# Kernel optimization log

Hardware: AMD Instinct MI355X
Metric: run time of the kernel (lower is better)

The kernel has to match this reference:

```python
import jax, jax.numpy as jnp
import numpy as np

H2 = 450
W = 1242
H = 375
N_PTS = 4_000_000


def setup_inputs() -> dict:
    key = jax.random.key(0)
    k1, k2, k3, k4, k5 = jax.random.split(key, 5)
    # lidar point cloud in velodyne frame (homogeneous): x forward, y left, z up
    u = jax.random.uniform(k1, (N_PTS, 3), dtype=jnp.float32)
    x = u[:, 0] * 78.0 + 2.0           # 2..80 m forward
    y = (u[:, 1] - 0.5) * 40.0         # -20..20 m lateral
    z = (u[:, 2] - 0.5) * 4.0 - 1.0    # -3..1 m vertical
    velo = jnp.stack([x, y, z, jnp.ones_like(x)], axis=1)
    # KITTI-like padded 4x4 intrinsic
    intrinsic = jnp.array([[721.5, 0.0, 609.5, 0.0],
                           [0.0, 721.5, 172.8, 0.0],
                           [0.0, 0.0, 1.0, 0.0],
                           [0.0, 0.0, 0.0, 1.0]], dtype=jnp.float32)
    # cam extrinsic ~ identity with small stereo baseline translation
    camExtrinsic = jnp.eye(4, dtype=jnp.float32).at[0, 3].set(-0.06)
    # velodyne -> camera rigid transform
    R = jnp.array([[0.0, -1.0, 0.0],
                   [0.0, 0.0, -1.0],
                   [1.0, 0.0, 0.0]], dtype=jnp.float32)
    t = jnp.array([0.0, -0.08, -0.27], dtype=jnp.float32)
    lidarExtrinsic = jnp.eye(4, dtype=jnp.float32).at[:3, :3].set(R).at[:3, 3].set(t)
    d = jax.random.uniform(k2, (H2, W), dtype=jnp.float32) * 78.0 + 2.0
    sel = jax.random.uniform(k3, (H2, W), dtype=jnp.float32) > 0.3
    interp_depth = jnp.where(sel, d, 0.0)
    return {"velo": velo, "intrinsic": intrinsic, "camExtrinsic": camExtrinsic,
            "lidarExtrinsic": lidarExtrinsic, "interp_depth": interp_depth,
            "h": H, "w": W}


def reference(velo, intrinsic, camExtrinsic, lidarExtrinsic, interp_depth, h, w):
    h2, wd = interp_depth.shape
    n = velo.shape[0]
    f32 = interp_depth.dtype

    P_cam = intrinsic @ camExtrinsic      # 4x4 projection to camera image
    P_lid = intrinsic @ lidarExtrinsic    # 4x4 projection to lidar image

    # project points into camera image
    vp = velo @ P_cam.T                    # [N,4]
    vz = vp[:, 2]
    vx = vp[:, 0] / vz
    vy = vp[:, 1] / vz
    onimg = (velo[:, 0] > 0) & (vx > 0) & (vx < w) & (vy > 0) & (vy < h)

    # project points into lidar image
    nv = velo @ P_lid.T                    # [N,4]
    nz = nv[:, 2]
    nx = nv[:, 0] / nz
    ny = nv[:, 1] / nz
    rnx = jnp.round(nx).astype(jnp.int32)
    rny = jnp.round(ny).astype(jnp.int32)
    nval = (rnx >= 0) & (rnx < w) & (rny >= 0) & (rny < h2) & (nz > 0) & onimg

    # dense interp-depth backprojection / reprojection, [h2, w]
    xxx, yyy = jnp.meshgrid(jnp.arange(wd, dtype=f32), jnp.arange(h2, dtype=f32), indexing='xy')
    d = interp_depth
    pts = jnp.stack([xxx * d, yyy * d, d, jnp.ones_like(d)], axis=-1)  # [h2,w,4]
    M = P_cam @ jnp.linalg.inv(P_lid)
    pp = jnp.einsum('hwk,jk->hwj', pts, M)                              # [h2,w,4]
    ppz = pp[..., 2]
    ppz_safe = jnp.where(ppz != 0, ppz, 1.0)
    ppx = pp[..., 0] / ppz_safe
    ppy = pp[..., 1] / ppz_safe
    interp_vals = jnp.stack([xxx, yyy, d, ppx, ppy, ppz, jnp.zeros_like(d)], axis=-1)
    img = jnp.where((d > 0)[..., None], interp_vals, 0.0)               # [h2,w,7]

    # scatter lidar points (overwrites interp entries where both present)
    idxrec = jnp.arange(n, dtype=f32)
    pvals = jnp.stack([nx, ny, nz, vx, vy, vz, idxrec], axis=1)         # [N,7]
    y_safe = jnp.where(nval, rny, h2)                                   # OOB -> dropped
    img = img.at[y_safe, rnx].set(pvals, mode='drop')

    org_mask = jnp.zeros((h2, wd), dtype=f32).at[y_safe, rnx].set(1.0, mode='drop')
    # NOTE: the custom CUDA occlusion pass (LidarFilterCuda.lidar_denoise) is
    # not reproducible; reference keeps the pre-denoise mask (identity filter).
    noocc_mask = org_mask

    pt_idx = img[:, :, 6].astype(jnp.int32)
    keep = noocc_mask == 1
    fi_idx = jnp.where(keep, pt_idx, n)                                 # OOB -> dropped
    filterIndicator = jnp.zeros((n,), dtype=jnp.int32).at[fi_idx.reshape(-1)].set(1, mode='drop')

    return img, noocc_mask, org_mask, filterIndicator
```

## Files before the change

kernel.cpp:

```cpp
#include <hip/hip_runtime.h>

#define H2C 450
#define WC 1242
#define HC 375
#define NPTS 4000000
#define NPIX (H2C * WC)


__device__ __forceinline__ void mm4(float* o, const float* a, const float* b) {
    for (int i = 0; i < 4; i++)
        for (int j = 0; j < 4; j++) {
            float t = a[i * 4 + 0] * b[0 * 4 + j];
            t = fmaf(a[i * 4 + 1], b[1 * 4 + j], t);
            t = fmaf(a[i * 4 + 2], b[2 * 4 + j], t);
            t = fmaf(a[i * 4 + 3], b[3 * 4 + j], t);
            o[i * 4 + j] = t;
        }
}

__global__ void setup_k(const float* __restrict__ K, const float* __restrict__ C,
                        const float* __restrict__ L, float* __restrict__ mats) {
#pragma clang fp contract(off)
    if (threadIdx.x != 0 || blockIdx.x != 0) return;
    float Pc[16], Pl[16], A[16], X[16], M[16];
    mm4(Pc, K, C);
    mm4(Pl, K, L);
    for (int i = 0; i < 16; i++) A[i] = Pl[i];
    int piv[4];
    for (int k = 0; k < 4; k++) {
        int p = k; float mx = fabsf(A[k * 4 + k]);
        for (int i = k + 1; i < 4; i++) { float v = fabsf(A[i * 4 + k]); if (v > mx) { mx = v; p = i; } }
        piv[k] = p;
        if (p != k) for (int j = 0; j < 4; j++) { float t = A[k * 4 + j]; A[k * 4 + j] = A[p * 4 + j]; A[p * 4 + j] = t; }
        float akk = A[k * 4 + k];
        if (fabsf(akk) >= 1.17549435e-38f) {
            float r = 1.0f / akk;
            for (int i = k + 1; i < 4; i++) A[i * 4 + k] = A[i * 4 + k] * r;
        } else {
            for (int i = k + 1; i < 4; i++) A[i * 4 + k] = A[i * 4 + k] / akk;
        }
        for (int i = k + 1; i < 4; i++) {
            float lik = A[i * 4 + k];
            for (int j = k + 1; j < 4; j++) A[i * 4 + j] = A[i * 4 + j] - lik * A[k * 4 + j];
        }
    }
    for (int i = 0; i < 16; i++) X[i] = 0.0f;
    X[0] = X[5] = X[10] = X[15] = 1.0f;
    for (int k = 0; k < 4; k++) if (piv[k] != k)
        for (int j = 0; j < 4; j++) { float t = X[k * 4 + j]; X[k * 4 + j] = X[piv[k] * 4 + j]; X[piv[k] * 4 + j] = t; }
    for (int j = 0; j < 4; j++) {
        for (int k = 0; k < 4; k++) {
            float xk = X[k * 4 + j];
            for (int i = k + 1; i < 4; i++) X[i * 4 + j] = X[i * 4 + j] - xk * A[i * 4 + k];
        }
        for (int k = 3; k >= 0; k--) {
            float xk = X[k * 4 + j] / A[k * 4 + k];
            X[k * 4 + j] = xk;
            for (int i = 0; i < k; i++) X[i * 4 + j] = X[i * 4 + j] - xk * A[i * 4 + k];
        }
    }
    mm4(M, Pc, X);
    for (int i = 0; i < 16; i++) { mats[i] = Pc[i]; mats[16 + i] = Pl[i]; mats[32 + i] = M[i]; }
}

__global__ void init_k(float4* __restrict__ fi4, int4* __restrict__ winner4) {
    int i = blockIdx.x * blockDim.x + threadIdx.x;
    if (i < NPTS / 4) fi4[i] = make_float4(0.f, 0.f, 0.f, 0.f);
    if (i < NPIX / 4) winner4[i] = make_int4(-1, -1, -1, -1);
}

__global__ void point_k(const float4* __restrict__ velo, const float* __restrict__ mats,
                        int* __restrict__ winner) {
    int i = blockIdx.x * blockDim.x + threadIdx.x;
    if (i >= NPTS) return;
    float4 v = velo[i];
    const float* Pc = mats;
    const float* Pl = mats + 16;
    float vp0 = fmaf(v.w, Pc[3],  fmaf(v.z, Pc[2],  fmaf(v.y, Pc[1], v.x * Pc[0])));
    float vp1 = fmaf(v.w, Pc[7],  fmaf(v.z, Pc[6],  fmaf(v.y, Pc[5], v.x * Pc[4])));
    float vz  = fmaf(v.w, Pc[11], fmaf(v.z, Pc[10], fmaf(v.y, Pc[9], v.x * Pc[8])));
    float vx = vp0 / vz;
    float vy = vp1 / vz;
    bool onimg = (v.x > 0.f) && (vx > 0.f) && (vx < (float)WC) && (vy > 0.f) && (vy < (float)HC);
    float nv0 = fmaf(v.w, Pl[3],  fmaf(v.z, Pl[2],  fmaf(v.y, Pl[1], v.x * Pl[0])));
    float nv1 = fmaf(v.w, Pl[7],  fmaf(v.z, Pl[6],  fmaf(v.y, Pl[5], v.x * Pl[4])));
    float nz  = fmaf(v.w, Pl[11], fmaf(v.z, Pl[10], fmaf(v.y, Pl[9], v.x * Pl[8])));
    float nx = nv0 / nz;
    float ny = nv1 / nz;
    float rx = rintf(nx);
    float ry = rintf(ny);
    if (onimg && (nz > 0.f) && (rx >= 0.f) && (rx < (float)WC) && (ry >= 0.f) && (ry < (float)H2C)) {
        int px = (int)rx, py = (int)ry;
        atomicMax(&winner[py * WC + px], i);
    }
}

__global__ void resolve_k(const float* __restrict__ depth, const float4* __restrict__ velo,
                          const float* __restrict__ mats, const int* __restrict__ winner,
                          float* __restrict__ img, float* __restrict__ noocc,
                          float* __restrict__ org, float* __restrict__ fi) {
#pragma clang fp contract(off)
    int p = blockIdx.x * blockDim.x + threadIdx.x;
    if (p >= NPIX) return;
    int wi = winner[p];
    float o0, o1, o2, o3, o4, o5, o6;
    if (wi >= 0) {
        float4 v = velo[wi];
        const float* Pc = mats;
        const float* Pl = mats + 16;
        float vp0 = fmaf(v.w, Pc[3],  fmaf(v.z, Pc[2],  fmaf(v.y, Pc[1], v.x * Pc[0])));
        float vp1 = fmaf(v.w, Pc[7],  fmaf(v.z, Pc[6],  fmaf(v.y, Pc[5], v.x * Pc[4])));
        float vz  = fmaf(v.w, Pc[11], fmaf(v.z, Pc[10], fmaf(v.y, Pc[9], v.x * Pc[8])));
        float nv0 = fmaf(v.w, Pl[3],  fmaf(v.z, Pl[2],  fmaf(v.y, Pl[1], v.x * Pl[0])));
        float nv1 = fmaf(v.w, Pl[7],  fmaf(v.z, Pl[6],  fmaf(v.y, Pl[5], v.x * Pl[4])));
        float nz  = fmaf(v.w, Pl[11], fmaf(v.z, Pl[10], fmaf(v.y, Pl[9], v.x * Pl[8])));
        o0 = nv0 / nz; o1 = nv1 / nz; o2 = nz;
        o3 = vp0 / vz; o4 = vp1 / vz; o5 = vz;
        o6 = (float)wi;
        noocc[p] = 1.0f;
        org[p] = 1.0f;
        fi[wi] = 1.0f;
    } else {
        noocc[p] = 0.0f;
        org[p] = 0.0f;
        float d = depth[p];
        if (d > 0.0f) {
            int y = p / WC, x = p - y * WC;
            float fx = (float)x, fy = (float)y;
            const float* M = mats + 32;
            float p0 = fx * d, p1 = fy * d;
            float pp0 = ((p0 * M[0] + p1 * M[1]) + d * M[2]) + M[3];
            float pp1 = ((p0 * M[4] + p1 * M[5]) + d * M[6]) + M[7];
            float pp2 = ((p0 * M[8] + p1 * M[9]) + d * M[10]) + M[11];
            float zs = (pp2 != 0.0f) ? pp2 : 1.0f;
            o0 = fx; o1 = fy; o2 = d;
            o3 = pp0 / zs; o4 = pp1 / zs; o5 = pp2;
            o6 = 0.0f;
        } else {
            o0 = o1 = o2 = o3 = o4 = o5 = o6 = 0.0f;
        }
    }
    float* ip = img + (size_t)p * 7;
    ip[0] = o0; ip[1] = o1; ip[2] = o2; ip[3] = o3; ip[4] = o4; ip[5] = o5; ip[6] = o6;
}

extern "C" void kernel_launch(void* const* d_in, const int* in_sizes, int n_in,
                              void* d_out, int out_size, void* d_ws, size_t ws_size,
                              hipStream_t stream) {
    const float* velo  = (const float*)d_in[0];
    const float* K     = (const float*)d_in[1];
    const float* C     = (const float*)d_in[2];
    const float* L     = (const float*)d_in[3];
    const float* depth = (const float*)d_in[4];

    float* out   = (float*)d_out;
    float* img   = out;
    float* noocc = out + (size_t)NPIX * 7;
    float* org   = noocc + NPIX;
    float* fi    = org + NPIX;

    float* mats  = (float*)d_ws;
    int* winner  = (int*)((char*)d_ws + 256);

    setup_k<<<1, 64, 0, stream>>>(K, C, L, mats);

    int initN = NPTS / 4;
    init_k<<<(initN + 255) / 256, 256, 0, stream>>>((float4*)fi, (int4*)winner);

    point_k<<<(NPTS + 255) / 256, 256, 0, stream>>>((const float4*)velo, mats, winner);

    resolve_k<<<(NPIX + 255) / 256, 256, 0, stream>>>(depth, (const float4*)velo, mats, winner,
                                                      img, noocc, org, fi);
}
```

Measured before the change: 33.62 us.

## Fuse init into setup/point kernels and stage img writes through shared memory

Merges the matrix setup kernel with winner-buffer initialisation, and moves zeroing of the filter indicator into the point projection kernel. This drops one launch and one separate 16 MB zeroing pass. The resolve kernel now stages each thread's 7-float record in shared memory and writes the block's output contiguously, so the stride-7 stores become coalesced. The costs are an extra barrier and shared-memory traffic per block, and each thread in the point kernel now issues an additional store.

After: 28.80 us. -14.4%, faster.

```diff
diff --git a/kernel.cpp b/kernel.cpp
--- a/kernel.cpp
+++ b/kernel.cpp
@@ -18,61 +18,59 @@
         }
 }
 
-__global__ void setup_k(const float* __restrict__ K, const float* __restrict__ C,
-                        const float* __restrict__ L, float* __restrict__ mats) {
+__global__ void init_mats_k(const float* __restrict__ K, const float* __restrict__ C,
+                            const float* __restrict__ L, float* __restrict__ mats,
+                            int4* __restrict__ winner4) {
 #pragma clang fp contract(off)
-    if (threadIdx.x != 0 || blockIdx.x != 0) return;
+    int i = blockIdx.x * blockDim.x + threadIdx.x;
+    if (i < NPIX / 4) winner4[i] = make_int4(-1, -1, -1, -1);
+    if (i != 0) return;
     float Pc[16], Pl[16], A[16], X[16], M[16];
     mm4(Pc, K, C);
     mm4(Pl, K, L);
-    for (int i = 0; i < 16; i++) A[i] = Pl[i];
+    for (int k = 0; k < 16; k++) A[k] = Pl[k];
     int piv[4];
     for (int k = 0; k < 4; k++) {
         int p = k; float mx = fabsf(A[k * 4 + k]);
-        for (int i = k + 1; i < 4; i++) { float v = fabsf(A[i * 4 + k]); if (v > mx) { mx = v; p = i; } }
+        for (int r = k + 1; r < 4; r++) { float v = fabsf(A[r * 4 + k]); if (v > mx) { mx = v; p = r; } }
         piv[k] = p;
         if (p != k) for (int j = 0; j < 4; j++) { float t = A[k * 4 + j]; A[k * 4 + j] = A[p * 4 + j]; A[p * 4 + j] = t; }
         float akk = A[k * 4 + k];
         if (fabsf(akk) >= 1.17549435e-38f) {
             float r = 1.0f / akk;
-            for (int i = k + 1; i < 4; i++) A[i * 4 + k] = A[i * 4 + k] * r;
+            for (int r2 = k + 1; r2 < 4; r2++) A[r2 * 4 + k] = A[r2 * 4 + k] * r;
         } else {
-            for (int i = k + 1; i < 4; i++) A[i * 4 + k] = A[i * 4 + k] / akk;
+            for (int r2 = k + 1; r2 < 4; r2++) A[r2 * 4 + k] = A[r2 * 4 + k] / akk;
         }
-        for (int i = k + 1; i < 4; i++) {
-            float lik = A[i * 4 + k];
-            for (int j = k + 1; j < 4; j++) A[i * 4 + j] = A[i * 4 + j] - lik * A[k * 4 + j];
+        for (int r = k + 1; r < 4; r++) {
+            float lik = A[r * 4 + k];
+            for (int j = k + 1; j < 4; j++) A[r * 4 + j] = A[r * 4 + j] - lik * A[k * 4 + j];
         }
     }
-    for (int i = 0; i < 16; i++) X[i] = 0.0f;
+    for (int k = 0; k < 16; k++) X[k] = 0.0f;
     X[0] = X[5] = X[10] = X[15] = 1.0f;
     for (int k = 0; k < 4; k++) if (piv[k] != k)
         for (int j = 0; j < 4; j++) { float t = X[k * 4 + j]; X[k * 4 + j] = X[piv[k] * 4 + j]; X[piv[k] * 4 + j] = t; }
     for (int j = 0; j < 4; j++) {
         for (int k = 0; k < 4; k++) {
             float xk = X[k * 4 + j];
-            for (int i = k + 1; i < 4; i++) X[i * 4 + j] = X[i * 4 + j] - xk * A[i * 4 + k];
+            for (int r = k + 1; r < 4; r++) X[r * 4 + j] = X[r * 4 + j] - xk * A[r * 4 + k];
         }
         for (int k = 3; k >= 0; k--) {
             float xk = X[k * 4 + j] / A[k * 4 + k];
             X[k * 4 + j] = xk;
-            for (int i = 0; i < k; i++) X[i * 4 + j] = X[i * 4 + j] - xk * A[i * 4 + k];
+            for (int r = 0; r < k; r++) X[r * 4 + j] = X[r * 4 + j] - xk * A[r * 4 + k];
         }
     }
     mm4(M, Pc, X);
-    for (int i = 0; i < 16; i++) { mats[i] = Pc[i]; mats[16 + i] = Pl[i]; mats[32 + i] = M[i]; }
-}
-
-__global__ void init_k(float4* __restrict__ fi4, int4* __restrict__ winner4) {
-    int i = blockIdx.x * blockDim.x + threadIdx.x;
-    if (i < NPTS / 4) fi4[i] = make_float4(0.f, 0.f, 0.f, 0.f);
-    if (i < NPIX / 4) winner4[i] = make_int4(-1, -1, -1, -1);
+    for (int k = 0; k < 16; k++) { mats[k] = Pc[k]; mats[16 + k] = Pl[k]; mats[32 + k] = M[k]; }
 }
 
 __global__ void point_k(const float4* __restrict__ velo, const float* __restrict__ mats,
-                        int* __restrict__ winner) {
+                        int* __restrict__ winner, float* __restrict__ fi) {
     int i = blockIdx.x * blockDim.x + threadIdx.x;
     if (i >= NPTS) return;
+    fi[i] = 0.0f;
     float4 v = velo[i];
     const float* Pc = mats;
     const float* Pl = mats + 16;
@@ -95,53 +93,60 @@
     }
 }
 
-__global__ void resolve_k(const float* __restrict__ depth, const float4* __restrict__ velo,
-                          const float* __restrict__ mats, const int* __restrict__ winner,
-                          float* __restrict__ img, float* __restrict__ noocc,
-                          float* __restrict__ org, float* __restrict__ fi) {
+__global__ void __launch_bounds__(256)
+resolve_k(const float* __restrict__ depth, const float4* __restrict__ velo,
+          const float* __restrict__ mats, const int* __restrict__ winner,
+          float* __restrict__ img, float* __restrict__ noocc,
+          float* __restrict__ org, float* __restrict__ fi) {
 #pragma clang fp contract(off)
-    int p = blockIdx.x * blockDim.x + threadIdx.x;
-    if (p >= NPIX) return;
-    int wi = winner[p];
-    float o0, o1, o2, o3, o4, o5, o6;
-    if (wi >= 0) {
-        float4 v = velo[wi];
-        const float* Pc = mats;
-        const float* Pl = mats + 16;
-        float vp0 = fmaf(v.w, Pc[3],  fmaf(v.z, Pc[2],  fmaf(v.y, Pc[1], v.x * Pc[0])));
-        float vp1 = fmaf(v.w, Pc[7],  fmaf(v.z, Pc[6],  fmaf(v.y, Pc[5], v.x * Pc[4])));
-        float vz  = fmaf(v.w, Pc[11], fmaf(v.z, Pc[10], fmaf(v.y, Pc[9], v.x * Pc[8])));
-        float nv0 = fmaf(v.w, Pl[3],  fmaf(v.z, Pl[2],  fmaf(v.y, Pl[1], v.x * Pl[0])));
-        float nv1 = fmaf(v.w, Pl[7],  fmaf(v.z, Pl[6],  fmaf(v.y, Pl[5], v.x * Pl[4])));
-        float nz  = fmaf(v.w, Pl[11], fmaf(v.z, Pl[10], fmaf(v.y, Pl[9], v.x * Pl[8])));
-        o0 = nv0 / nz; o1 = nv1 / nz; o2 = nz;
-        o3 = vp0 / vz; o4 = vp1 / vz; o5 = vz;
-        o6 = (float)wi;
-        noocc[p] = 1.0f;
-        org[p] = 1.0f;
-        fi[wi] = 1.0f;
-    } else {
-        noocc[p] = 0.0f;
-        org[p] = 0.0f;
-        float d = depth[p];
-        if (d > 0.0f) {
-            int y = p / WC, x = p - y * WC;
-            float fx = (float)x, fy = (float)y;
-            const float* M = mats + 32;
-            float p0 = fx * d, p1 = fy * d;
-            float pp0 = ((p0 * M[0] + p1 * M[1]) + d * M[2]) + M[3];
-            float pp1 = ((p0 * M[4] + p1 * M[5]) + d * M[6]) + M[7];
-            float pp2 = ((p0 * M[8] + p1 * M[9]) + d * M[10]) + M[11];
-            float zs = (pp2 != 0.0f) ? pp2 : 1.0f;
-            o0 = fx; o1 = fy; o2 = d;
-            o3 = pp0 / zs; o4 = pp1 / zs; o5 = pp2;
-            o6 = 0.0f;
+    __shared__ float srec[256 * 7];
+    int pb = blockIdx.x * 256;
+    int p = pb + threadIdx.x;
+    int valid = NPIX - pb; if (valid > 256) valid = 256;
+    float o0 = 0.f, o1 = 0.f, o2 = 0.f, o3 = 0.f, o4 = 0.f, o5 = 0.f, o6 = 0.f;
+    if (p < NPIX) {
+        int wi = winner[p];
+        if (wi >= 0) {
+            float4 v = velo[wi];
+            const float* Pc = mats;
+            const float* Pl = mats + 16;
+            float vp0 = fmaf(v.w, Pc[3],  fmaf(v.z, Pc[2],  fmaf(v.y, Pc[1], v.x * Pc[0])));
+            float vp1 = fmaf(v.w, Pc[7],  fmaf(v.z, Pc[6],  fmaf(v.y, Pc[5], v.x * Pc[4])));
+            float vz  = fmaf(v.w, Pc[11], fmaf(v.z, Pc[10], fmaf(v.y, Pc[9], v.x * Pc[8])));
+            float nv0 = fmaf(v.w, Pl[3],  fmaf(v.z, Pl[2],  fmaf(v.y, Pl[1], v.x * Pl[0])));
+            float nv1 = fmaf(v.w, Pl[7],  fmaf(v.z, Pl[6],  fmaf(v.y, Pl[5], v.x * Pl[4])));
+            float nz  = fmaf(v.w, Pl[11], fmaf(v.z, Pl[10], fmaf(v.y, Pl[9], v.x * Pl[8])));
+            o0 = nv0 / nz; o1 = nv1 / nz; o2 = nz;
+            o3 = vp0 / vz; o4 = vp1 / vz; o5 = vz;
+            o6 = (float)wi;
+            noocc[p] = 1.0f;
+            org[p] = 1.0f;
+            fi[wi] = 1.0f;
         } else {
-            o0 = o1 = o2 = o3 = o4 = o5 = o6 = 0.0f;
+            noocc[p] = 0.0f;
+            org[p] = 0.0f;
+            float d = depth[p];
+            if (d > 0.0f) {
+                int y = p / WC, x = p - y * WC;
+                float fx = (float)x, fy = (float)y;
+                const float* M = mats + 32;
+                float p0 = fx * d, p1 = fy * d;
+                float pp0 = ((p0 * M[0] + p1 * M[1]) + d * M[2]) + M[3];
+                float pp1 = ((p0 * M[4] + p1 * M[5]) + d * M[6]) + M[7];
+                float pp2 = ((p0 * M[8] + p1 * M[9]) + d * M[10]) + M[11];
+                float zs = (pp2 != 0.0f) ? pp2 : 1.0f;
+                o0 = fx; o1 = fy; o2 = d;
+                o3 = pp0 / zs; o4 = pp1 / zs; o5 = pp2;
+                o6 = 0.0f;
+            }
         }
     }
-    float* ip = img + (size_t)p * 7;
-    ip[0] = o0; ip[1] = o1; ip[2] = o2; ip[3] = o3; ip[4] = o4; ip[5] = o5; ip[6] = o6;
+    float* r = srec + threadIdx.x * 7;
+    r[0] = o0; r[1] = o1; r[2] = o2; r[3] = o3; r[4] = o4; r[5] = o5; r[6] = o6;
+    __syncthreads();
+    float* obase = img + (size_t)pb * 7;
+    int nfl = valid * 7;
+    for (int k = threadIdx.x; k < nfl; k += 256) obase[k] = srec[k];
 }
 
 extern "C" void kernel_launch(void* const* d_in, const int* in_sizes, int n_in,
@@ -162,12 +167,9 @@
     float* mats  = (float*)d_ws;
     int* winner  = (int*)((char*)d_ws + 256);
 
-    setup_k<<<1, 64, 0, stream>>>(K, C, L, mats);
+    init_mats_k<<<(NPIX / 4 + 255) / 256, 256, 0, stream>>>(K, C, L, mats, (int4*)winner);
 
-    int initN = NPTS / 4;
-    init_k<<<(initN + 255) / 256, 256, 0, stream>>>((float4*)fi, (int4*)winner);
-
-    point_k<<<(NPTS + 255) / 256, 256, 0, stream>>>((const float4*)velo, mats, winner);
+    point_k<<<(NPTS + 255) / 256, 256, 0, stream>>>((const float4*)velo, mats, winner, fi);
 
     resolve_k<<<(NPIX + 255) / 256, 256, 0, stream>>>(depth, (const float4*)velo, mats, winner,
                                                       img, noocc, org, fi);
```
